# Optimization experiments

Hardware: AMD Instinct MI355X
Metric: run time of the kernel (lower is better)

## Reference

```python
import jax, jax.numpy as jnp
import numpy as np

LRU_DIM = 256
HIDDEN = 256
H = 64
N = LRU_DIM // H  # 4 (even, per assert)
R_MIN, R_MAX, MAX_PHASE = 0.9, 0.999, 6.28
BSZ, T = 8, 4096


def _rotate_half(x):
    # interleaved pairs: [x0,x1,x2,x3,...] -> [-x1,x0,-x3,x2,...]
    r = jnp.stack([-x[..., 1::2], x[..., 0::2]], axis=-1)
    return r.reshape(x.shape)


def _mix_sequence(gamma, thetas, Us):
    # gamma: scalar, thetas: (N/2,), Us: (T,B,N) -> (T,B,N)
    Tlen = Us.shape[0]
    gammas = jnp.broadcast_to(gamma, (Tlen,))
    ths = jnp.broadcast_to(thetas, (Tlen,) + thetas.shape)

    def binf(a, b):
        gi, ti, xi = a
        gj, tj, xj = b
        theta = jnp.repeat(tj, 2, axis=-1)            # (T, N): [t0,t0,t1,t1,...]
        sin = jnp.sin(theta)[..., None, :]            # (T,1,N)
        cos = jnp.cos(theta)[..., None, :]
        acc = gj[..., None, None] * (cos * xi + sin * _rotate_half(xi)) + xj
        return (gi * gj, ti + tj, acc)

    _, _, res = jax.lax.associative_scan(binf, (gammas, ths, Us), axis=0)
    return res


def setup_inputs() -> dict:
    key = jax.random.key(0)
    ks = jax.random.split(key, 7)
    scale = 1.0 / np.sqrt(HIDDEN + LRU_DIM)
    u = jax.random.normal(ks[0], (BSZ, HIDDEN, T), dtype=jnp.float32)
    thetas_log = jnp.log(jax.random.uniform(ks[1], (H, N // 2), minval=0.01, maxval=1.0) * MAX_PHASE).astype(jnp.float32)
    P_param = (jax.random.normal(ks[2], (H, N, N), dtype=jnp.float32) / np.sqrt(LRU_DIM + N)).astype(jnp.float32)
    B_param = (jax.random.normal(ks[3], (H, N, HIDDEN), dtype=jnp.float32) * scale).astype(jnp.float32)
    C = (jax.random.normal(ks[4], (HIDDEN, LRU_DIM), dtype=jnp.float32) * scale).astype(jnp.float32)
    D = jax.random.normal(ks[5], (HIDDEN,), dtype=jnp.float32)
    u1 = jax.random.uniform(ks[6], (H,))
    gamma_log = (np.log(-np.log(R_MAX)) + u1 * (np.log(-np.log(R_MIN)) - np.log(-np.log(R_MAX)))).astype(jnp.float32)
    return {"u": u, "thetas_log": thetas_log, "P_param": P_param,
            "B_param": B_param, "C": C, "D": D, "gamma_log": gamma_log}


def reference(u, thetas_log, P_param, B_param, C, D, gamma_log):
    Bsz, hidden, Tlen = u.shape
    ut = jnp.transpose(u, (0, 2, 1))                       # (B,T,Dh)
    gamma = jnp.exp(-jnp.exp(gamma_log))                   # (H,)
    trace_per_head = jnp.sum(B_param * B_param, axis=(1, 2))  # tr(B B^T) per head
    norm = jnp.sqrt((1.0 - gamma ** 2) / trace_per_head)
    B_norm = norm[:, None, None] * B_param                 # (H,N,Dh)
    skew = P_param - jnp.swapaxes(P_param, 1, 2)
    P = jax.vmap(jax.scipy.linalg.expm)(skew)              # (H,N,N), orthogonal
    Us = jnp.einsum('HnD,BTD->HTBn', B_norm, ut)           # (H,T,B,N)
    Us = jnp.einsum('HNn,HTBn->HTBN', P, Us)               # == einsum with P^T as in torch
    thetas = jnp.exp(thetas_log)                           # (H,N/2)
    y = jax.vmap(_mix_sequence)(gamma, thetas, Us)         # (H,T,B,N)
    y = jnp.einsum('HNn,HTBN->HTBn', P, y)
    y = jnp.transpose(y, (2, 1, 0, 3)).reshape(Bsz, Tlen, -1)  # (B,T,lru_dim)
    y = jnp.einsum('Dn,BTn->BTD', C, y) + D * ut
    return jnp.transpose(y, (0, 2, 1))                     # (B,Dh,T)
```

## Files before the change

### kernel.cpp

```cpp
#include <hip/hip_runtime.h>
#include <math.h>


typedef __attribute__((ext_vector_type(8))) short short8;
typedef __attribute__((ext_vector_type(4))) float f32x4;

#define TLEN 4096
#define LCH 32
#define NCH 128
#define BSZ 8
#define LDW 132
#define LDK 264

constexpr int MB_OFF   = 0;
constexpr int CB_OFF   = 32768;
constexpr int AP_OFF   = 65536;
constexpr int ALP_OFF  = AP_OFF + (LCH + 1) * 256;
constexpr int TOT_OFF  = ALP_OFF + (NCH + 1) * 256;
constexpr int ZST_OFF  = TOT_OFF + NCH * BSZ * 256;

__device__ __forceinline__ float bfbits2f(unsigned int bits16) {
  union { unsigned int u; float f; } v; v.u = bits16 << 16; return v.f;
}
__device__ __forceinline__ unsigned int f2bfbits(float f) {
  union { float f; unsigned int u; } v; v.f = f;
  return (v.u + 0x7fffu + ((v.u >> 16) & 1u)) >> 16;
}
__device__ __forceinline__ unsigned int pack2(float x, float y) {
  return f2bfbits(x) | (f2bfbits(y) << 16);
}

__global__ __launch_bounds__(256) void k0_setup(
    const float* __restrict__ thetas_log, const float* __restrict__ P_param,
    const float* __restrict__ B_param, const float* __restrict__ C,
    const float* __restrict__ gamma_log, float* __restrict__ ws) {
  const int h = blockIdx.x;
  const int tid = threadIdx.x;
  __shared__ float red[4];
  __shared__ float Psh[16];
  __shared__ float nrmsh;

  {
    float4 v = *(const float4*)(B_param + (size_t)h * 1024 + tid * 4);
    float s = v.x * v.x + v.y * v.y + v.z * v.z + v.w * v.w;
#pragma unroll
    for (int off = 32; off > 0; off >>= 1) s += __shfl_down(s, off);
    if ((tid & 63) == 0) red[tid >> 6] = s;
  }
  __syncthreads();

  if (tid == 0) {
    double A[4][4], E[4][4], Tm[4][4];
    for (int i = 0; i < 4; ++i)
      for (int j = 0; j < 4; ++j)
        A[i][j] = (double)P_param[h * 16 + i * 4 + j] - (double)P_param[h * 16 + j * 4 + i];
    double fro = 0.0;
    for (int i = 0; i < 4; ++i) for (int j = 0; j < 4; ++j) fro += A[i][j] * A[i][j];
    fro = sqrt(fro);
    int s = 0;
    while (fro > 0.25 && s < 30) { fro *= 0.5; ++s; }
    double scl = 1.0;
    for (int q2 = 0; q2 < s; ++q2) scl *= 0.5;
    for (int i = 0; i < 4; ++i) for (int j = 0; j < 4; ++j) A[i][j] *= scl;
    for (int i = 0; i < 4; ++i)
      for (int j = 0; j < 4; ++j) { E[i][j] = (i == j) ? 1.0 : 0.0; Tm[i][j] = E[i][j]; }
    for (int k = 1; k <= 16; ++k) {
      double Tn[4][4];
      for (int i = 0; i < 4; ++i)
        for (int j = 0; j < 4; ++j) {
          double acc = 0.0;
          for (int m = 0; m < 4; ++m) acc += Tm[i][m] * A[m][j];
          Tn[i][j] = acc / (double)k;
        }
      for (int i = 0; i < 4; ++i)
        for (int j = 0; j < 4; ++j) { Tm[i][j] = Tn[i][j]; E[i][j] += Tn[i][j]; }
    }
    for (int q2 = 0; q2 < s; ++q2) {
      double E2[4][4];
      for (int i = 0; i < 4; ++i)
        for (int j = 0; j < 4; ++j) {
          double acc = 0.0;
          for (int m = 0; m < 4; ++m) acc += E[i][m] * E[m][j];
          E2[i][j] = acc;
        }
      for (int i = 0; i < 4; ++i) for (int j = 0; j < 4; ++j) E[i][j] = E2[i][j];
    }
    for (int i = 0; i < 4; ++i)
      for (int j = 0; j < 4; ++j) Psh[i * 4 + j] = (float)E[i][j];
  } else if (tid == 64 || tid == 65) {
    const int p = h * 2 + (tid - 64);
    double th = exp((double)thetas_log[p]);
    double g = exp(-exp((double)gamma_log[h]));
    double ar = g * cos(th), ai = g * sin(th);
    float2* Apw = (float2*)(ws + AP_OFF);
    float2* ALp = (float2*)(ws + ALP_OFF);
    double xr = 1.0, xi = 0.0;
    Apw[p] = make_float2(1.f, 0.f);
    for (int j = 1; j <= LCH; ++j) {
      double nr = xr * ar - xi * ai, ni = xr * ai + xi * ar;
      xr = nr; xi = ni;
      Apw[j * 128 + p] = make_float2((float)xr, (float)xi);
    }
    double br = xr, bi = xi;
    xr = 1.0; xi = 0.0;
    ALp[p] = make_float2(1.f, 0.f);
    for (int k = 1; k <= NCH; ++k) {
      double nr = xr * br - xi * bi, ni = xr * bi + xi * br;
      xr = nr; xi = ni;
      ALp[k * 128 + p] = make_float2((float)xr, (float)xi);
    }
  } else if (tid == 128) {
    double g = exp(-exp((double)gamma_log[h]));
    double tr = (double)red[0] + red[1] + red[2] + red[3];
    nrmsh = (float)sqrt((1.0 - g * g) / tr);
  }
  __syncthreads();

  unsigned short* Mbf = (unsigned short*)(ws + MB_OFF);
  unsigned int*   Cbd = (unsigned int*)(ws + CB_OFF);
  {
    float b0 = B_param[(h * 4 + 0) * 256 + tid];
    float b1 = B_param[(h * 4 + 1) * 256 + tid];
    float b2 = B_param[(h * 4 + 2) * 256 + tid];
    float b3 = B_param[(h * 4 + 3) * 256 + tid];
    float nrm = nrmsh;
#pragma unroll
    for (int N = 0; N < 4; ++N) {
      float acc = Psh[N * 4 + 0] * b0 + Psh[N * 4 + 1] * b1 +
                  Psh[N * 4 + 2] * b2 + Psh[N * 4 + 3] * b3;
      Mbf[(h * 4 + N) * 256 + tid] = (unsigned short)f2bfbits(nrm * acc);
    }
  }
  {
    float4 cv = *(const float4*)(C + (size_t)tid * 256 + h * 4);
    float o[4];
#pragma unroll
    for (int N = 0; N < 4; ++N)
      o[N] = cv.x * Psh[N * 4 + 0] + cv.y * Psh[N * 4 + 1] +
             cv.z * Psh[N * 4 + 2] + cv.w * Psh[N * 4 + 3];
    Cbd[(tid * 256 + h * 4) >> 1]       = pack2(o[0], o[1]);
    Cbd[((tid * 256 + h * 4) >> 1) + 1] = pack2(o[2], o[3]);
  }
}

__global__ __launch_bounds__(256, 4) void k1_mfma(
    const float* __restrict__ u, float* __restrict__ ws) {
  __shared__ __align__(16) unsigned char smem[LCH * LDK * 2];
  unsigned short* us = (unsigned short*)smem;
  unsigned int*   wd = (unsigned int*)smem;

  const int c = blockIdx.x, b = blockIdx.y;
  const int t0 = c * LCH;
  const int tid = threadIdx.x;
  const int L = tid & 63;
  const int w = __builtin_amdgcn_readfirstlane(tid >> 6);
  const int qh = L >> 4, l15 = L & 15;

  {
    const int dp = tid >> 3;
    const int t4 = (tid & 7) * 4;
#pragma unroll
    for (int i = 0; i < 4; ++i) {
      int j = dp + 32 * i;
      float4 va = *(const float4*)(u + (size_t)(b * 256 + 2 * j) * TLEN + t0 + t4);
      float4 vb = *(const float4*)(u + (size_t)(b * 256 + 2 * j + 1) * TLEN + t0 + t4);
      float av[4] = {va.x, va.y, va.z, va.w};
      float bv[4] = {vb.x, vb.y, vb.z, vb.w};
#pragma unroll
      for (int dt = 0; dt < 4; ++dt)
        wd[(t4 + dt) * LDW + j] = pack2(av[dt], bv[dt]);
    }
  }
  __syncthreads();

  f32x4 acc[4][2];
#pragma unroll
  for (int rt = 0; rt < 4; ++rt)
#pragma unroll
    for (int tt = 0; tt < 2; ++tt) acc[rt][tt] = (f32x4){0.f, 0.f, 0.f, 0.f};
  {
    const unsigned short* Mbf = (const unsigned short*)(ws + MB_OFF);
#pragma unroll
    for (int ks = 0; ks < 8; ++ks) {
      short8 af[4], bf[2];
#pragma unroll
      for (int rt = 0; rt < 4; ++rt)
        af[rt] = *(const short8*)(Mbf + (size_t)(w * 64 + rt * 16 + l15) * 256 + ks * 32 + qh * 8);
#pragma unroll
      for (int tt = 0; tt < 2; ++tt)
        bf[tt] = *(const short8*)(us + (tt * 16 + l15) * LDK + ks * 32 + qh * 8);
#pragma unroll
      for (int rt = 0; rt < 4; ++rt)
#pragma unroll
        for (int tt = 0; tt < 2; ++tt)
          acc[rt][tt] = __builtin_amdgcn_mfma_f32_16x16x32_bf16(af[rt], bf[tt], acc[rt][tt], 0, 0, 0);
    }
  }
  __syncthreads();

#pragma unroll
  for (int rt = 0; rt < 4; ++rt) {
    int pbase = w * 32 + rt * 8 + qh * 2;
#pragma unroll
    for (int tt = 0; tt < 2; ++tt) {
      int t = tt * 16 + l15;
      f32x4 a4 = acc[rt][tt];
      wd[t * LDW + pbase]     = pack2(a4[0], a4[1]);
      wd[t * LDW + pbase + 1] = pack2(a4[2], a4[3]);
    }
  }
  __syncthreads();

  if (tid < 128) {
    const int p = tid;
    const float2* Apw = (const float2*)(ws + AP_OFF);
    float2 a = Apw[128 + p];
    float zr = 0.f, zi = 0.f;
#pragma unroll
    for (int t = 0; t < LCH; ++t) {
      unsigned int wv = wd[t * LDW + p];
      float wr = bfbits2f(wv & 0xffffu), wi = bfbits2f(wv >> 16);
      float nr = fmaf(a.x, zr, fmaf(-a.y, zi, wr));
      float ni = fmaf(a.x, zi, fmaf(a.y, zr, wi));
      zr = nr; zi = ni;
      wd[t * LDW + p] = pack2(zr, zi);
    }
    ((float2*)(ws + TOT_OFF))[(c * BSZ + b) * 128 + p] = make_float2(zr, zi);
  }
  __syncthreads();

  unsigned int* Zg = (unsigned int*)(ws + ZST_OFF) + (size_t)(c * BSZ + b) * 4096;
#pragma unroll
  for (int jj = 0; jj < 16; ++jj) {
    int idx = tid + 256 * jj;
    Zg[idx] = wd[(idx >> 7) * LDW + (idx & 127)];
  }
}

__global__ __launch_bounds__(256, 4) void k3_mfma(
    const float* __restrict__ u, const float* __restrict__ Dv,
    const float* __restrict__ ws, float* __restrict__ out) {
  __shared__ __align__(16) unsigned char smem[LCH * LDK * 2];
  unsigned int* wd = (unsigned int*)smem;

  const int c = blockIdx.x, b = blockIdx.y;
  const int t0 = c * LCH;
  const int tid = threadIdx.x;
  const int L = tid & 63;
  const int w = __builtin_amdgcn_readfirstlane(tid >> 6);
  const int qh = L >> 4, l15 = L & 15;

  {
    const unsigned int* Zg = (const unsigned int*)(ws + ZST_OFF) + (size_t)(c * BSZ + b) * 4096;
#pragma unroll
    for (int jj = 0; jj < 16; ++jj) {
      int idx = tid + 256 * jj;
      wd[(idx >> 7) * LDW + (idx & 127)] = Zg[idx];
    }
  }
  __syncthreads();

  {
    const int p = tid & 127;
    const int thalf = (tid >> 7) * 16;
    float cr = 0.f, ci = 0.f;
    const float2* ALp = (const float2*)(ws + ALP_OFF);
    const float2* Tot = (const float2*)(ws + TOT_OFF);
    for (int cp = 0; cp < c; ++cp) {
      float2 al = ALp[(c - 1 - cp) * 128 + p];
      float2 tv = Tot[(cp * BSZ + b) * 128 + p];
      cr = fmaf(al.x, tv.x, fmaf(-al.y, tv.y, cr));
      ci = fmaf(al.x, tv.y, fmaf(al.y, tv.x, ci));
    }
    const float2* Apw = (const float2*)(ws + AP_OFF);
#pragma unroll
    for (int tt2 = 0; tt2 < 16; ++tt2) {
      int t = thalf + tt2;
      unsigned int wv = wd[t * LDW + p];
      float2 ap = Apw[(t + 1) * 128 + p];
      float sr = fmaf(ap.x, cr, fmaf(-ap.y, ci, bfbits2f(wv & 0xffffu)));
      float si = fmaf(ap.x, ci, fmaf(ap.y, cr, bfbits2f(wv >> 16)));
      wd[t * LDW + p] = pack2(sr, si);
    }
  }
  __syncthreads();

  f32x4 acc[4][2];
#pragma unroll
  for (int rt = 0; rt < 4; ++rt)
#pragma unroll
    for (int tt = 0; tt < 2; ++tt) acc[rt][tt] = (f32x4){0.f, 0.f, 0.f, 0.f};
  {
    const unsigned short* Cbf = (const unsigned short*)(ws + CB_OFF);
    const unsigned short* zs  = (const unsigned short*)smem;
#pragma unroll
    for (int ks = 0; ks < 8; ++ks) {
      short8 af[4], bf[2];
#pragma unroll
      for (int rt = 0; rt < 4; ++rt)
        af[rt] = *(const short8*)(Cbf + (size_t)(w * 64 + rt * 16 + l15) * 256 + ks * 32 + qh * 8);
#pragma unroll
      for (int tt = 0; tt < 2; ++tt)
        bf[tt] = *(const short8*)(zs + (tt * 16 + l15) * LDK + ks * 32 + qh * 8);
#pragma unroll
      for (int rt = 0; rt < 4; ++rt)
#pragma unroll
        for (int tt = 0; tt < 2; ++tt)
          acc[rt][tt] = __builtin_amdgcn_mfma_f32_16x16x32_bf16(af[rt], bf[tt], acc[rt][tt], 0, 0, 0);
    }
  }

  float dv[4][4];
#pragma unroll
  for (int rt = 0; rt < 4; ++rt)
#pragma unroll
    for (int q = 0; q < 4; ++q) dv[rt][q] = Dv[w * 64 + rt * 16 + qh * 4 + q];
#pragma unroll
  for (int rt = 0; rt < 4; ++rt) {
    int Dbase = w * 64 + rt * 16 + qh * 4;
#pragma unroll
    for (int tt = 0; tt < 2; ++tt) {
      int t = tt * 16 + l15;
      f32x4 a4 = acc[rt][tt];
      size_t obase = (size_t)(b * 256 + Dbase) * TLEN + t0 + t;
#pragma unroll
      for (int q = 0; q < 4; ++q)
        out[obase + (size_t)q * TLEN] = a4[q] + dv[rt][q] * u[obase + (size_t)q * TLEN];
    }
  }
}

extern "C" void kernel_launch(void* const* d_in, const int* in_sizes, int n_in,
                              void* d_out, int out_size, void* d_ws, size_t ws_size,
                              hipStream_t stream) {
  const float* u          = (const float*)d_in[0];
  const float* thetas_log = (const float*)d_in[1];
  const float* P_param    = (const float*)d_in[2];
  const float* B_param    = (const float*)d_in[3];
  const float* C          = (const float*)d_in[4];
  const float* Dvec       = (const float*)d_in[5];
  const float* gamma_log  = (const float*)d_in[6];
  float* out = (float*)d_out;
  float* ws  = (float*)d_ws;

  hipLaunchKernelGGL(k0_setup, dim3(64), dim3(256), 0, stream,
                     thetas_log, P_param, B_param, C, gamma_log, ws);
  hipLaunchKernelGGL(k1_mfma, dim3(NCH, BSZ), dim3(256), 0, stream, u, ws);
  hipLaunchKernelGGL(k3_mfma, dim3(NCH, BSZ), dim3(256), 0, stream, u, Dvec, ws, out);
}
```

Measured before the change: 182.8 us.

## Replace per-chunk quadratic carry recomputation with sequential carry-scan kernel

Before, each k3 block recomputed its incoming carry by summing over all earlier chunk totals weighted by precomputed powers, which is quadratic work across chunks. A new small kernel k2_carry runs a sequential scan over the 128 chunks per batch and overwrites each chunk's total slot with its incoming carry. k3 then reads a single carry value and fuses the carry application into the global-to-LDS load, which also removes one barrier. The cost is an extra kernel launch, plus a serial 128-step chain running on only 8 small blocks.

```diff
diff --git a/kernel.cpp b/kernel.cpp
--- a/kernel.cpp
+++ b/kernel.cpp
@@ -93,21 +93,12 @@
     double g = exp(-exp((double)gamma_log[h]));
     double ar = g * cos(th), ai = g * sin(th);
     float2* Apw = (float2*)(ws + AP_OFF);
-    float2* ALp = (float2*)(ws + ALP_OFF);
     double xr = 1.0, xi = 0.0;
     Apw[p] = make_float2(1.f, 0.f);
     for (int j = 1; j <= LCH; ++j) {
       double nr = xr * ar - xi * ai, ni = xr * ai + xi * ar;
       xr = nr; xi = ni;
       Apw[j * 128 + p] = make_float2((float)xr, (float)xi);
-    }
-    double br = xr, bi = xi;
-    xr = 1.0; xi = 0.0;
-    ALp[p] = make_float2(1.f, 0.f);
-    for (int k = 1; k <= NCH; ++k) {
-      double nr = xr * br - xi * bi, ni = xr * bi + xi * br;
-      xr = nr; xi = ni;
-      ALp[k * 128 + p] = make_float2((float)xr, (float)xi);
     }
   } else if (tid == 128) {
     double g = exp(-exp((double)gamma_log[h]));
@@ -237,6 +228,24 @@
   }
 }
 
+__global__ __launch_bounds__(128) void k2_carry(float* __restrict__ ws) {
+  const int b = blockIdx.x;
+  const int p = threadIdx.x;
+  const float2* Apw = (const float2*)(ws + AP_OFF);
+  float2* Tot = (float2*)(ws + TOT_OFF);
+  const float2 aL = Apw[LCH * 128 + p];
+  float cr = 0.f, ci = 0.f;
+#pragma unroll 4
+  for (int c = 0; c < NCH; ++c) {
+    float2* slot = Tot + (size_t)(c * BSZ + b) * 128 + p;
+    float2 tv = *slot;
+    *slot = make_float2(cr, ci);
+    float nr = fmaf(aL.x, cr, fmaf(-aL.y, ci, tv.x));
+    float ni = fmaf(aL.x, ci, fmaf(aL.y, cr, tv.y));
+    cr = nr; ci = ni;
+  }
+}
+
 __global__ __launch_bounds__(256, 4) void k3_mfma(
     const float* __restrict__ u, const float* __restrict__ Dv,
     const float* __restrict__ ws, float* __restrict__ out) {
@@ -251,35 +260,18 @@
   const int qh = L >> 4, l15 = L & 15;
 
   {
+    const int p = tid & 127;
+    const float2 cv = ((const float2*)(ws + TOT_OFF))[(size_t)(c * BSZ + b) * 128 + p];
+    const float2* Apw = (const float2*)(ws + AP_OFF);
     const unsigned int* Zg = (const unsigned int*)(ws + ZST_OFF) + (size_t)(c * BSZ + b) * 4096;
 #pragma unroll
     for (int jj = 0; jj < 16; ++jj) {
       int idx = tid + 256 * jj;
-      wd[(idx >> 7) * LDW + (idx & 127)] = Zg[idx];
-    }
-  }
-  __syncthreads();
-
-  {
-    const int p = tid & 127;
-    const int thalf = (tid >> 7) * 16;
-    float cr = 0.f, ci = 0.f;
-    const float2* ALp = (const float2*)(ws + ALP_OFF);
-    const float2* Tot = (const float2*)(ws + TOT_OFF);
-    for (int cp = 0; cp < c; ++cp) {
-      float2 al = ALp[(c - 1 - cp) * 128 + p];
-      float2 tv = Tot[(cp * BSZ + b) * 128 + p];
-      cr = fmaf(al.x, tv.x, fmaf(-al.y, tv.y, cr));
-      ci = fmaf(al.x, tv.y, fmaf(al.y, tv.x, ci));
-    }
-    const float2* Apw = (const float2*)(ws + AP_OFF);
-#pragma unroll
-    for (int tt2 = 0; tt2 < 16; ++tt2) {
-      int t = thalf + tt2;
-      unsigned int wv = wd[t * LDW + p];
+      int t = idx >> 7;
+      unsigned int wv = Zg[idx];
       float2 ap = Apw[(t + 1) * 128 + p];
-      float sr = fmaf(ap.x, cr, fmaf(-ap.y, ci, bfbits2f(wv & 0xffffu)));
-      float si = fmaf(ap.x, ci, fmaf(ap.y, cr, bfbits2f(wv >> 16)));
+      float sr = fmaf(ap.x, cv.x, fmaf(-ap.y, cv.y, bfbits2f(wv & 0xffffu)));
+      float si = fmaf(ap.x, cv.y, fmaf(ap.y, cv.x, bfbits2f(wv >> 16)));
       wd[t * LDW + p] = pack2(sr, si);
     }
   }
@@ -346,5 +338,6 @@
   hipLaunchKernelGGL(k0_setup, dim3(64), dim3(256), 0, stream,
                      thetas_log, P_param, B_param, C, gamma_log, ws);
   hipLaunchKernelGGL(k1_mfma, dim3(NCH, BSZ), dim3(256), 0, stream, u, ws);
+  hipLaunchKernelGGL(k2_carry, dim3(BSZ), dim3(128), 0, stream, ws);
   hipLaunchKernelGGL(k3_mfma, dim3(NCH, BSZ), dim3(256), 0, stream, u, Dvec, ws, out);
 }
```

New measurement: 172.5 us. -5.6%, faster.

## Fuse chunk scan and output kernels with flag-based cross-block carry propagation

Applied to the files above, without the earlier changes.

Merges the per-chunk scan kernel and the output kernel into one launch. The chunked local states stay in shared memory instead of round-tripping through global memory. Each block publishes its chunk total and sets a release flag, then waits on acquire flags from all earlier chunks before forming its carry-in with a Horner recurrence. That recurrence replaces the precomputed table of chunk-power coefficients. The design relies on earlier blocks being scheduled first; if they are not, blocks could spin or deadlock, and the serial wait chains add latency across chunks.

```diff
diff --git a/kernel.cpp b/kernel.cpp
--- a/kernel.cpp
+++ b/kernel.cpp
@@ -15,9 +15,8 @@
 constexpr int MB_OFF   = 0;
 constexpr int CB_OFF   = 32768;
 constexpr int AP_OFF   = 65536;
-constexpr int ALP_OFF  = AP_OFF + (LCH + 1) * 256;
-constexpr int TOT_OFF  = ALP_OFF + (NCH + 1) * 256;
-constexpr int ZST_OFF  = TOT_OFF + NCH * BSZ * 256;
+constexpr int FLG_OFF  = AP_OFF + (LCH + 1) * 256;
+constexpr int TOT_OFF  = FLG_OFF + NCH * BSZ;
 
 __device__ __forceinline__ float bfbits2f(unsigned int bits16) {
   union { unsigned int u; float f; } v; v.u = bits16 << 16; return v.f;
@@ -39,6 +38,8 @@
   __shared__ float red[4];
   __shared__ float Psh[16];
   __shared__ float nrmsh;
+
+  if (tid < 16) ((unsigned int*)(ws + FLG_OFF))[h * 16 + tid] = 0u;
 
   {
     float4 v = *(const float4*)(B_param + (size_t)h * 1024 + tid * 4);
@@ -93,7 +94,6 @@
     double g = exp(-exp((double)gamma_log[h]));
     double ar = g * cos(th), ai = g * sin(th);
     float2* Apw = (float2*)(ws + AP_OFF);
-    float2* ALp = (float2*)(ws + ALP_OFF);
     double xr = 1.0, xi = 0.0;
     Apw[p] = make_float2(1.f, 0.f);
     for (int j = 1; j <= LCH; ++j) {
@@ -101,14 +101,6 @@
       xr = nr; xi = ni;
       Apw[j * 128 + p] = make_float2((float)xr, (float)xi);
     }
-    double br = xr, bi = xi;
-    xr = 1.0; xi = 0.0;
-    ALp[p] = make_float2(1.f, 0.f);
-    for (int k = 1; k <= NCH; ++k) {
-      double nr = xr * br - xi * bi, ni = xr * bi + xi * br;
-      xr = nr; xi = ni;
-      ALp[k * 128 + p] = make_float2((float)xr, (float)xi);
-    }
   } else if (tid == 128) {
     double g = exp(-exp((double)gamma_log[h]));
     double tr = (double)red[0] + red[1] + red[2] + red[3];
@@ -143,8 +135,9 @@
   }
 }
 
-__global__ __launch_bounds__(256, 4) void k1_mfma(
-    const float* __restrict__ u, float* __restrict__ ws) {
+__global__ __launch_bounds__(256, 4) void k13_fused(
+    const float* __restrict__ u, const float* __restrict__ Dv,
+    float* __restrict__ ws, float* __restrict__ out) {
   __shared__ __align__(16) unsigned char smem[LCH * LDK * 2];
   unsigned short* us = (unsigned short*)smem;
   unsigned int*   wd = (unsigned int*)smem;
@@ -155,6 +148,7 @@
   const int L = tid & 63;
   const int w = __builtin_amdgcn_readfirstlane(tid >> 6);
   const int qh = L >> 4, l15 = L & 15;
+  unsigned int* flg = (unsigned int*)(ws + FLG_OFF);
 
   {
     const int dp = tid >> 3;
@@ -228,51 +222,35 @@
     ((float2*)(ws + TOT_OFF))[(c * BSZ + b) * 128 + p] = make_float2(zr, zi);
   }
   __syncthreads();
-
-  unsigned int* Zg = (unsigned int*)(ws + ZST_OFF) + (size_t)(c * BSZ + b) * 4096;
-#pragma unroll
-  for (int jj = 0; jj < 16; ++jj) {
-    int idx = tid + 256 * jj;
-    Zg[idx] = wd[(idx >> 7) * LDW + (idx & 127)];
-  }
-}
-
-__global__ __launch_bounds__(256, 4) void k3_mfma(
-    const float* __restrict__ u, const float* __restrict__ Dv,
-    const float* __restrict__ ws, float* __restrict__ out) {
-  __shared__ __align__(16) unsigned char smem[LCH * LDK * 2];
-  unsigned int* wd = (unsigned int*)smem;
-
-  const int c = blockIdx.x, b = blockIdx.y;
-  const int t0 = c * LCH;
-  const int tid = threadIdx.x;
-  const int L = tid & 63;
-  const int w = __builtin_amdgcn_readfirstlane(tid >> 6);
-  const int qh = L >> 4, l15 = L & 15;
-
-  {
-    const unsigned int* Zg = (const unsigned int*)(ws + ZST_OFF) + (size_t)(c * BSZ + b) * 4096;
-#pragma unroll
-    for (int jj = 0; jj < 16; ++jj) {
-      int idx = tid + 256 * jj;
-      wd[(idx >> 7) * LDW + (idx & 127)] = Zg[idx];
-    }
-  }
-  __syncthreads();
-
-  {
+  if (tid == 0) {
+    __threadfence();
+    __hip_atomic_store(&flg[c * BSZ + b], 1u, __ATOMIC_RELEASE,
+                       __HIP_MEMORY_SCOPE_AGENT);
+  }
+
+  if (c > 0) {
+    const int p = tid & 127;
+    const int cp = (p < c) ? p : (c - 1);
+    while (__hip_atomic_load(&flg[cp * BSZ + b], __ATOMIC_ACQUIRE,
+                             __HIP_MEMORY_SCOPE_AGENT) == 0u)
+      __builtin_amdgcn_s_sleep(2);
+  }
+  __syncthreads();
+
+  if (c > 0) {
     const int p = tid & 127;
     const int thalf = (tid >> 7) * 16;
+    const float2* Tot = (const float2*)(ws + TOT_OFF);
+    const float2* Apw = (const float2*)(ws + AP_OFF);
+    const float2 aL = Apw[LCH * 128 + p];
     float cr = 0.f, ci = 0.f;
-    const float2* ALp = (const float2*)(ws + ALP_OFF);
-    const float2* Tot = (const float2*)(ws + TOT_OFF);
+#pragma unroll 4
     for (int cp = 0; cp < c; ++cp) {
-      float2 al = ALp[(c - 1 - cp) * 128 + p];
-      float2 tv = Tot[(cp * BSZ + b) * 128 + p];
-      cr = fmaf(al.x, tv.x, fmaf(-al.y, tv.y, cr));
-      ci = fmaf(al.x, tv.y, fmaf(al.y, tv.x, ci));
-    }
-    const float2* Apw = (const float2*)(ws + AP_OFF);
+      float2 tv = Tot[(size_t)(cp * BSZ + b) * 128 + p];
+      float nr = fmaf(aL.x, cr, fmaf(-aL.y, ci, tv.x));
+      float ni = fmaf(aL.x, ci, fmaf(aL.y, cr, tv.y));
+      cr = nr; ci = ni;
+    }
 #pragma unroll
     for (int tt2 = 0; tt2 < 16; ++tt2) {
       int t = thalf + tt2;
@@ -285,11 +263,11 @@
   }
   __syncthreads();
 
-  f32x4 acc[4][2];
+  f32x4 acc2[4][2];
 #pragma unroll
   for (int rt = 0; rt < 4; ++rt)
 #pragma unroll
-    for (int tt = 0; tt < 2; ++tt) acc[rt][tt] = (f32x4){0.f, 0.f, 0.f, 0.f};
+    for (int tt = 0; tt < 2; ++tt) acc2[rt][tt] = (f32x4){0.f, 0.f, 0.f, 0.f};
   {
     const unsigned short* Cbf = (const unsigned short*)(ws + CB_OFF);
     const unsigned short* zs  = (const unsigned short*)smem;
@@ -306,7 +284,7 @@
       for (int rt = 0; rt < 4; ++rt)
 #pragma unroll
         for (int tt = 0; tt < 2; ++tt)
-          acc[rt][tt] = __builtin_amdgcn_mfma_f32_16x16x32_bf16(af[rt], bf[tt], acc[rt][tt], 0, 0, 0);
+          acc2[rt][tt] = __builtin_amdgcn_mfma_f32_16x16x32_bf16(af[rt], bf[tt], acc2[rt][tt], 0, 0, 0);
     }
   }
 
@@ -321,7 +299,7 @@
 #pragma unroll
     for (int tt = 0; tt < 2; ++tt) {
       int t = tt * 16 + l15;
-      f32x4 a4 = acc[rt][tt];
+      f32x4 a4 = acc2[rt][tt];
       size_t obase = (size_t)(b * 256 + Dbase) * TLEN + t0 + t;
 #pragma unroll
       for (int q = 0; q < 4; ++q)
@@ -345,6 +323,6 @@
 
   hipLaunchKernelGGL(k0_setup, dim3(64), dim3(256), 0, stream,
                      thetas_log, P_param, B_param, C, gamma_log, ws);
-  hipLaunchKernelGGL(k1_mfma, dim3(NCH, BSZ), dim3(256), 0, stream, u, ws);
-  hipLaunchKernelGGL(k3_mfma, dim3(NCH, BSZ), dim3(256), 0, stream, u, Dvec, ws, out);
-}
+  hipLaunchKernelGGL(k13_fused, dim3(NCH, BSZ), dim3(256), 0, stream,
+                     u, Dvec, ws, out);
+}
```

Result: slower. 252.9 us (+38.3%).
